# Kernel tuning notes

Hardware: AMD Instinct MI355X
Metric: run time of the kernel (lower is better)

## Reference

```python
import jax, jax.numpy as jnp
import numpy as np

EPS = 1e-5  # RMSNorm epsilon


def rmsnorm(x, w):
    return x * jax.lax.rsqrt(jnp.mean(x * x, axis=-1, keepdims=True) + EPS) * w


def mamba_forward(u, in_proj_w, conv_w, conv_b, x_proj_w, dt_proj_w, dt_proj_b,
                  A_log, D_param, mamba_out_w):
    # u: (b, L, dm) -- canonical Mamba block (expand=2, d_state=16, d_conv=4)
    b, L, dm = u.shape
    di, ds = A_log.shape
    dtr = dt_proj_w.shape[1]
    xz = jnp.einsum('bld,ed->ble', u, in_proj_w)          # (b,L,2*di)
    x_, z = jnp.split(xz, 2, axis=-1)                     # each (b,L,di)
    # causal depthwise conv over the sequence axis
    dconv = conv_w.shape[-1]
    xc = jnp.transpose(x_, (0, 2, 1))                     # (b,di,L)
    xc = jnp.pad(xc, ((0, 0), (0, 0), (dconv - 1, 0)))
    xc = jax.lax.conv_general_dilated(xc, conv_w, window_strides=(1,), padding='VALID',
                                      dimension_numbers=('NCH', 'OIH', 'NCH'),
                                      feature_group_count=di)
    xc = xc + conv_b[None, :, None]
    x_ = jax.nn.silu(jnp.transpose(xc, (0, 2, 1)))        # (b,L,di)
    # input-dependent dt, B, C
    x_dbl = jnp.einsum('bld,ed->ble', x_, x_proj_w)       # (b,L,dtr+2*ds)
    dt, B, C = jnp.split(x_dbl, [dtr, dtr + ds], axis=-1)
    delta = jax.nn.softplus(jnp.einsum('blr,dr->bld', dt, dt_proj_w) + dt_proj_b)  # (b,L,di)
    A = -jnp.exp(A_log)                                   # (di,ds)

    def step(h, inp):
        d_t, B_t, C_t, x_t = inp                          # (b,di),(b,ds),(b,ds),(b,di)
        dA = jnp.exp(d_t[:, :, None] * A)                 # (b,di,ds)
        h = dA * h + (d_t * x_t)[:, :, None] * B_t[:, None, :]
        y = jnp.einsum('bds,bs->bd', h, C_t)
        return h, y

    xs = (jnp.moveaxis(delta, 1, 0), jnp.moveaxis(B, 1, 0),
          jnp.moveaxis(C, 1, 0), jnp.moveaxis(x_, 1, 0))
    h0 = jnp.zeros((b, di, ds), dtype=u.dtype)
    _, ys = jax.lax.scan(step, h0, xs)                    # ys: (L,b,di)
    y = jnp.moveaxis(ys, 0, 1) + x_ * D_param             # (b,L,di)
    y = y * jax.nn.silu(z)
    return jnp.einsum('bld,od->blo', y, mamba_out_w)      # (b,L,dm)


def conv1x1(W, bvec, t):
    # t: (b, cin, L) -> (b, cout, L)
    return jnp.einsum('oi,bit->bot', W, t) + bvec[None, :, None]


def reference(x, w_norm1, w_norm2, W_ip, b_ip, W_fp, b_fp, W_wp, b_wp, W_op, b_op,
              in_proj_w, conv_w, conv_b, x_proj_w, dt_proj_w, dt_proj_b,
              A_log, D_param, mamba_out_w):
    # x: (b, L, D) -- module's (b, c, l) with l == input_dim = D, c == seq = L
    residual = x
    xn = rmsnorm(x, w_norm1)                 # RMSNorm over last (input_dim) axis
    xt = jnp.transpose(xn, (0, 2, 1))        # 'b c l -> b l c' : (b, D, L)
    ssm = conv1x1(W_ip, b_ip, xt)            # (b, 2D, L)
    ssm = conv1x1(W_fp, b_fp, ssm)           # (b, 2D, L)
    u = jnp.transpose(ssm, (0, 2, 1))        # (b, L, 2D): seq=L, d_model=2D
    m = mamba_forward(u, in_proj_w, conv_w, conv_b, x_proj_w, dt_proj_w, dt_proj_b,
                      A_log, D_param, mamba_out_w)
    m = rmsnorm(m, w_norm2) + u              # PostNormMamba residual
    ssm = jnp.transpose(m, (0, 2, 1))        # (b, 2D, L)
    w = conv1x1(W_wp, b_wp, xt)              # (b, 2D, L)
    w = w * jax.nn.sigmoid(w)                # swish
    out = conv1x1(W_op, b_op, w * ssm)       # (b, D, L)
    return jnp.transpose(out, (0, 2, 1)) + residual


def setup_inputs():
    key = jax.random.key(0)
    ks = jax.random.split(key, 16)
    D, L, b = 64, 4096, 4
    dm, di, ds, dconv = 2 * D, 4 * D, 16, 4
    dtr = (dm + 15) // 16  # dt_rank = ceil(d_model/16) = 8

    def n(k, shape, fan_in):
        return jax.random.normal(k, shape, jnp.float32) * (1.0 / np.sqrt(fan_in))

    return {
        'x': jax.random.normal(ks[0], (b, L, D), jnp.float32),
        'w_norm1': jnp.ones((D,), jnp.float32),
        'w_norm2': jnp.ones((dm,), jnp.float32),
        'W_ip': n(ks[1], (2 * D, D), D), 'b_ip': jnp.zeros((2 * D,), jnp.float32),
        'W_fp': n(ks[2], (2 * D, 2 * D), 2 * D), 'b_fp': jnp.zeros((2 * D,), jnp.float32),
        'W_wp': n(ks[3], (2 * D, D), D), 'b_wp': jnp.zeros((2 * D,), jnp.float32),
        'W_op': n(ks[4], (D, 2 * D), 2 * D), 'b_op': jnp.zeros((D,), jnp.float32),
        'in_proj_w': n(ks[5], (2 * di, dm), dm),
        'conv_w': n(ks[6], (di, 1, dconv), dconv),
        'conv_b': jnp.zeros((di,), jnp.float32),
        'x_proj_w': n(ks[7], (dtr + 2 * ds, di), di),
        'dt_proj_w': n(ks[8], (di, dtr), dtr),
        'dt_proj_b': jnp.full((di,), float(np.log(np.expm1(0.01))), jnp.float32),
        'A_log': jnp.log(jnp.broadcast_to(jnp.arange(1, ds + 1, dtype=jnp.float32), (di, ds))),
        'D_param': jnp.ones((di,), jnp.float32),
        'mamba_out_w': n(ks[9], (dm, di), di),
    }
```

## Files before the change

### kernel.cpp

```cpp
#include <hip/hip_runtime.h>
#include <hip/hip_bf16.h>

typedef __hip_bfloat16 bf16;
typedef __attribute__((ext_vector_type(8))) short bf16x8;
typedef __attribute__((ext_vector_type(4))) float f32x4;
#define DEV __device__ __forceinline__

constexpr int SEQ  = 4096;
constexpr int NB   = 4;
constexpr int NTOK = NB * SEQ;
constexpr float EPS = 1e-5f;
constexpr int NCH = 64;
constexpr int NCHUNK = SEQ / NCH;
constexpr float LOG2E = 1.44269504f;

constexpr int OFF_WDT  = 0;
constexpr int OFF_WB   = 2048;
constexpr int WB_IP = 0;
constexpr int WB_WP = 8192;
constexpr int WB_FP = 16384;
constexpr int WB_PR = 32768;
constexpr int WB_MO = 98304;
constexpr int WB_OP = 131072;
constexpr int WB_XP = 139264;
constexpr int WB_TOT = 151552;
constexpr int OFF_XDBL = OFF_WB + WB_TOT / 2;
constexpr int OFF_R1   = OFF_XDBL + NTOK * 40;
constexpr int OFF_WSW  = OFF_R1   + 1048576;
constexpr int OFF_U    = OFF_WSW  + 1048576;
constexpr int OFF_R2   = OFF_U    + 1048576;
constexpr int OFF_SILUZ= OFF_R2   + 2097152;
constexpr int OFF_XC   = OFF_SILUZ+ 2097152;
constexpr int OFF_G    = OFF_XC   + 2097152;
constexpr int OFF_FLAG = OFF_G    + 2097152;

DEV float b2f(bf16 x) { return __bfloat162float(x); }
DEV bf16 f2b(float x) { return __float2bfloat16(x); }
DEV short shof(bf16 h) { short s; __builtin_memcpy(&s, &h, 2); return s; }
DEV float ldin(const void* p, int i, int f) {
  return f ? ((const float*)p)[i] : b2f(((const bf16*)p)[i]);
}
DEV unsigned pack2(float a, float b) {
  bf16 ha = f2b(a), hb = f2b(b);
  unsigned short ua, ub;
  __builtin_memcpy(&ua, &ha, 2); __builtin_memcpy(&ub, &hb, 2);
  return (unsigned)ua | ((unsigned)ub << 16);
}
DEV float lo16f(unsigned u) { return __int_as_float((int)(u << 16)); }
DEV float hi16f(unsigned u) { return __int_as_float((int)(u & 0xffff0000u)); }
template<int CTRL>
DEV float dpp_add(float v) {
  int r = __builtin_amdgcn_update_dpp(0, __float_as_int(v), CTRL, 0xF, 0xF, false);
  return v + __int_as_float(r);
}
DEV float exp2f_fast(float a) { return __builtin_amdgcn_exp2f(a); }
DEV float softplus(float a) {
  return (a > 20.f) ? a : __logf(1.f + exp2f_fast(a * LOG2E));
}
DEV float silu(float a) { return a / (1.f + __expf(-a)); }

DEV void cpw(int e, int base, int count, const void* __restrict__ src,
             bf16* __restrict__ wb, int f) {
  int r = e - base;
  if (r >= 0 && r < count) wb[base + r] = f2b(ldin(src, r, f));
}
__global__ __launch_bounds__(256) void prep_k(
    const void* __restrict__ w_ip, const void* __restrict__ w_wp, const void* __restrict__ w_fp,
    const void* __restrict__ w_pr, const void* __restrict__ w_mo, const void* __restrict__ w_op,
    const void* __restrict__ w_x,  const void* __restrict__ w_dt,
    const void* __restrict__ x, float* __restrict__ wsf, int* __restrict__ flagp)
{
  __shared__ int cnt;
  if (threadIdx.x == 0) cnt = 0;
  __syncthreads();
  {
    float v = b2f(((const bf16*)x)[threadIdx.x]);
    int ok = (v == v) && fabsf(v) > 1e-4f && fabsf(v) < 100.f;
    atomicAdd(&cnt, ok);
  }
  __syncthreads();
  int f = (cnt > 204) ? 0 : 1;
  if (blockIdx.x == 0 && threadIdx.x == 0) *flagp = f;

  int e = blockIdx.x * 256 + threadIdx.x;
  bf16* wb = (bf16*)(wsf + OFF_WB);
  cpw(e, WB_IP, 8192,  w_ip, wb, f);
  cpw(e, WB_WP, 8192,  w_wp, wb, f);
  cpw(e, WB_FP, 16384, w_fp, wb, f);
  cpw(e, WB_PR, 65536, w_pr, wb, f);
  cpw(e, WB_MO, 32768, w_mo, wb, f);
  cpw(e, WB_OP, 8192,  w_op, wb, f);
  {
    int r = e - WB_XP;
    if (r >= 0 && r < 12288) wb[WB_XP + r] = (r < 10240) ? f2b(ldin(w_x, r, f)) : f2b(0.f);
  }
  if (e < 2048) {
    int r = e >> 8, d = e & 255;
    wsf[OFF_WDT + e] = ldin(w_dt, d * 8 + r, f);
  }
}

__global__ __launch_bounds__(256) void fm_k(
    const void* __restrict__ x, const void* __restrict__ w1, const float* __restrict__ wsf,
    const void* __restrict__ b_ip, const void* __restrict__ b_wp, const void* __restrict__ b_fp,
    bf16* __restrict__ wsw, bf16* __restrict__ u, bf16* __restrict__ xpre,
    bf16* __restrict__ siluz, const int* __restrict__ flagp)
{
  __shared__ short xn[32 * 72];
  __shared__ short t1[32 * 136];
  __shared__ short ul[32 * 136];
  const int f = *flagp;
  const int tid = threadIdx.x;
  const int tok0 = blockIdx.x * 32;
  {
    const int token = tid >> 3, r = tid & 7;
    float v[8]; float ss = 0.f;
    #pragma unroll
    for (int k = 0; k < 8; ++k) {
      v[k] = ldin(x, (tok0 + token) * 64 + r * 8 + k, f);
      ss += v[k] * v[k];
    }
    ss += __shfl_xor(ss, 1, 8); ss += __shfl_xor(ss, 2, 8); ss += __shfl_xor(ss, 4, 8);
    float sc = rsqrtf(ss * (1.f / 64.f) + EPS);
    unsigned* dst = (unsigned*)xn + token * 36 + r * 4;
    #pragma unroll
    for (int k = 0; k < 4; ++k) {
      int i = r * 8 + k * 2;
      dst[k] = pack2(v[k*2] * sc * ldin(w1, i, f), v[k*2+1] * sc * ldin(w1, i + 1, f));
    }
  }
  __syncthreads();
  const int lane = tid & 63, m = lane & 15, q = lane >> 4;
  const int w = tid >> 6;
  {
    const int wt = w >> 1, ng = w & 1;
    const bf16* W = (const bf16*)(wsf + OFF_WB) + (wt ? WB_WP : WB_IP);
    const void* bia = wt ? b_wp : b_ip;
    bf16x8 a[2][2];
    #pragma unroll
    for (int mt = 0; mt < 2; ++mt)
      #pragma unroll
      for (int kk = 0; kk < 2; ++kk)
        a[mt][kk] = *(const bf16x8*)&xn[(mt * 16 + m) * 72 + kk * 32 + q * 8];
    #pragma unroll
    for (int nti = 0; nti < 4; ++nti) {
      int nt = ng * 4 + nti;
      int n = nt * 16 + m;
      f32x4 acc[2] = {{0,0,0,0},{0,0,0,0}};
      #pragma unroll
      for (int kk = 0; kk < 2; ++kk) {
        bf16x8 b = *(const bf16x8*)(W + (nt * 16 + m) * 64 + kk * 32 + q * 8);
        #pragma unroll
        for (int mt = 0; mt < 2; ++mt)
          acc[mt] = __builtin_amdgcn_mfma_f32_16x16x32_bf16(a[mt][kk], b, acc[mt], 0, 0, 0);
      }
      float bv = ldin(bia, n, f);
      #pragma unroll
      for (int mt = 0; mt < 2; ++mt)
        #pragma unroll
        for (int r = 0; r < 4; ++r) {
          float v = acc[mt][r] + bv;
          if (wt) wsw[(tok0 + mt * 16 + q * 4 + r) * 128 + n] = f2b(silu(v));
          else    t1[(mt * 16 + q * 4 + r) * 136 + n] = shof(f2b(v));
        }
    }
  }
  __syncthreads();
  {
    const bf16* WF = (const bf16*)(wsf + OFF_WB) + WB_FP;
    bf16x8 a[2][4];
    #pragma unroll
    for (int mt = 0; mt < 2; ++mt)
      #pragma unroll
      for (int kk = 0; kk < 4; ++kk)
        a[mt][kk] = *(const bf16x8*)&t1[(mt * 16 + m) * 136 + kk * 32 + q * 8];
    #pragma unroll
    for (int nti = 0; nti < 2; ++nti) {
      int nt = w * 2 + nti;
      int n = nt * 16 + m;
      f32x4 acc[2] = {{0,0,0,0},{0,0,0,0}};
      #pragma unroll
      for (int kk = 0; kk < 4; ++kk) {
        bf16x8 b = *(const bf16x8*)(WF + (nt * 16 + m) * 128 + kk * 32 + q * 8);
        #pragma unroll
        for (int mt = 0; mt < 2; ++mt)
          acc[mt] = __builtin_amdgcn_mfma_f32_16x16x32_bf16(a[mt][kk], b, acc[mt], 0, 0, 0);
      }
      float bv = ldin(b_fp, n, f);
      #pragma unroll
      for (int mt = 0; mt < 2; ++mt)
        #pragma unroll
        for (int r = 0; r < 4; ++r) {
          bf16 h = f2b(acc[mt][r] + bv);
          ul[(mt * 16 + q * 4 + r) * 136 + n] = shof(h);
          u[(tok0 + mt * 16 + q * 4 + r) * 128 + n] = h;
        }
    }
  }
  __syncthreads();
  {
    const bf16* WP = (const bf16*)(wsf + OFF_WB) + WB_PR;
    bf16x8 a[2][4];
    #pragma unroll
    for (int mt = 0; mt < 2; ++mt)
      #pragma unroll
      for (int kk = 0; kk < 4; ++kk)
        a[mt][kk] = *(const bf16x8*)&ul[(mt * 16 + m) * 136 + kk * 32 + q * 8];
    #pragma unroll
    for (int nti = 0; nti < 8; ++nti) {
      int nt = w * 8 + nti;
      int n = nt * 16 + m;
      f32x4 acc[2] = {{0,0,0,0},{0,0,0,0}};
      #pragma unroll
      for (int kk = 0; kk < 4; ++kk) {
        bf16x8 b = *(const bf16x8*)(WP + (nt * 16 + m) * 128 + kk * 32 + q * 8);
        #pragma unroll
        for (int mt = 0; mt < 2; ++mt)
          acc[mt] = __builtin_amdgcn_mfma_f32_16x16x32_bf16(a[mt][kk], b, acc[mt], 0, 0, 0);
      }
      #pragma unroll
      for (int mt = 0; mt < 2; ++mt)
        #pragma unroll
        for (int r = 0; r < 4; ++r) {
          int tok = tok0 + mt * 16 + q * 4 + r;
          if (n < 256) xpre[tok * 256 + n] = f2b(acc[mt][r]);
          else         siluz[tok * 256 + (n - 256)] = f2b(silu(acc[mt][r]));
        }
    }
  }
}

__global__ __launch_bounds__(256) void conv_k(
    const bf16* __restrict__ xpre, const void* __restrict__ cw, const void* __restrict__ cb,
    const float* __restrict__ wsf, bf16* __restrict__ xc, float* __restrict__ xdbl,
    const int* __restrict__ flagp)
{
  __shared__ short xh[35 * 256];
  __shared__ short cs[32 * 264];
  const int f = *flagp;
  const int tid = threadIdx.x;
  const int tok0 = blockIdx.x * 32;
  const bool seqstart = (tok0 & (SEQ - 1)) == 0;
  for (int c = tid; c < 1120; c += 256) {
    int e0 = c * 8;
    int tt = e0 >> 8, i = e0 & 255;
    int gtok = tok0 + tt - 3;
    uint4* dst = (uint4*)(xh + e0);
    if (gtok >= 0 && !(seqstart && tt < 3)) *dst = *(const uint4*)(xpre + gtok * 256 + i);
    else                                    *dst = make_uint4(0, 0, 0, 0);
  }
  __syncthreads();
  {
    const int ch0 = (tid & 63) * 4;
    const int t0 = (tid >> 6) * 8;
    float w4[4][4], cb4[4];
    #pragma unroll
    for (int c = 0; c < 4; ++c) {
      cb4[c] = ldin(cb, ch0 + c, f);
      #pragma unroll
      for (int k = 0; k < 4; ++k) w4[c][k] = ldin(cw, (ch0 + c) * 4 + k, f);
    }
    float win[11][4];
    #pragma unroll
    for (int r = 0; r < 11; ++r) {
      uint2 v = *(const uint2*)&xh[(t0 + r) * 256 + ch0];
      win[r][0] = lo16f(v.x); win[r][1] = hi16f(v.x);
      win[r][2] = lo16f(v.y); win[r][3] = hi16f(v.y);
    }
    #pragma unroll
    for (int t = 0; t < 8; ++t) {
      unsigned pk[2];
      #pragma unroll
      for (int cp = 0; cp < 2; ++cp) {
        float o[2];
        #pragma unroll
        for (int ci = 0; ci < 2; ++ci) {
          int c = cp * 2 + ci;
          float acc = cb4[c];
          #pragma unroll
          for (int k = 0; k < 4; ++k) acc = fmaf(win[t + k][c], w4[c][k], acc);
          o[ci] = silu(acc);
        }
        pk[cp] = pack2(o[0], o[1]);
      }
      uint2 pv = make_uint2(pk[0], pk[1]);
      *(uint2*)&cs[(t0 + t) * 264 + ch0] = pv;
      *(uint2*)(xc + (tok0 + t0 + t) * 256 + ch0) = pv;
    }
  }
  __syncthreads();
  const int w = tid >> 6;
  if (w < 2) {
    const bf16* Wx = (const bf16*)(wsf + OFF_WB) + WB_XP;
    const int lane = tid & 63, m = lane & 15, quad = lane >> 4;
    f32x4 acc[3] = {{0,0,0,0},{0,0,0,0},{0,0,0,0}};
    #pragma unroll
    for (int k0 = 0; k0 < 256; k0 += 32) {
      bf16x8 af = *(const bf16x8*)&cs[(w * 16 + m) * 264 + k0 + quad * 8];
      #pragma unroll
      for (int nt = 0; nt < 3; ++nt) {
        bf16x8 bfr = *(const bf16x8*)(Wx + (nt * 16 + m) * 256 + k0 + quad * 8);
        acc[nt] = __builtin_amdgcn_mfma_f32_16x16x32_bf16(af, bfr, acc[nt], 0, 0, 0);
      }
    }
    #pragma unroll
    for (int nt = 0; nt < 3; ++nt) {
      int n = nt * 16 + m;
      if (n < 40) {
        #pragma unroll
        for (int r = 0; r < 4; ++r)
          xdbl[(tok0 + w * 16 + quad * 4 + r) * 40 + n] = acc[nt][r];
      }
    }
  }
}

template<bool IS_C>
__global__ __launch_bounds__(256) void scan_k(
    const float* __restrict__ xdbl, const bf16* __restrict__ xc, const bf16* __restrict__ siluz,
    const void* __restrict__ A_log, const void* __restrict__ D_par, const void* __restrict__ dt_b,
    const float* __restrict__ WDT, float* __restrict__ summ, const float* __restrict__ hinit,
    bf16* __restrict__ g, const int* __restrict__ flagp)
{
  const int f = *flagp;
  const int tid = threadIdx.x;
  const int bb = blockIdx.x >> 4, dg = blockIdx.x & 15, c = blockIdx.y;
  const int dl = tid >> 4, s = tid & 15;
  const int j = s;
  const int d_loop = dg * 16 + dl;
  const int d_stg  = dg * 16 + j;
  const int tok_base = bb * SEQ + c * NCH;

  __shared__ float dt_l[NCH * 8];
  __shared__ float dx_l[NCH * 16 * 2];
  __shared__ float bc_l[IS_C ? NCH * 16 * 2 : NCH * 16];
  __shared__ float g_l[IS_C ? NCH * 16 : 1];

  const float Aval2 = -__expf(ldin(A_log, d_loop * 16 + s, f)) * LOG2E;
  const float Dp_stg = ldin(D_par, d_stg, f);
  const float dtb_j = ldin(dt_b, d_stg, f);
  float wdt[8];
  #pragma unroll
  for (int r = 0; r < 8; ++r) wdt[r] = WDT[r * 256 + d_stg];

  const int sidx = (blockIdx.x * NCHUNK + c) * 256 + tid;
  float h = IS_C ? hinit[sidx] : 0.f;
  float sdlt = 0.f;

  for (int e2 = tid * 4; e2 < NCH * 8; e2 += 1024)
    *(float4*)(dt_l + e2) = *(const float4*)(xdbl + (tok_base + (e2 >> 3)) * 40 + (e2 & 7));
  #pragma unroll
  for (int k = 0; k < 4; ++k) {
    int e = tid + k * 256;
    int t = e >> 4;
    int tok = tok_base + t;
    float B = xdbl[tok * 40 + 8 + j];
    if (IS_C) {
      bc_l[e * 2 + 0] = B;
      bc_l[e * 2 + 1] = xdbl[tok * 40 + 24 + j];
    } else bc_l[e] = B;
  }
  __syncthreads();
  #pragma unroll
  for (int k = 0; k < 4; ++k) {
    int e = tid + k * 256;
    int t = e >> 4;
    float a = dtb_j;
    #pragma unroll
    for (int r = 0; r < 8; ++r) a = fmaf(dt_l[t * 8 + r], wdt[r], a);
    float dlt = softplus(a);
    float xcv = b2f(xc[(tok_base + t) * 256 + d_stg]);
    *(float2*)(dx_l + e * 2) = make_float2(dlt, dlt * xcv);
  }
  __syncthreads();

  #pragma unroll 8
  for (int t = 0; t < NCH; ++t) {
    float2 dx = *(const float2*)(dx_l + (t * 16 + dl) * 2);
    float dA = exp2f_fast(dx.x * Aval2);
    if (!IS_C) sdlt += dx.x;
    if (IS_C) {
      float2 bc = *(const float2*)(bc_l + (t * 16 + s) * 2);
      h = fmaf(dA, h, dx.y * bc.x);
      float p = h * bc.y;
      p = dpp_add<0x121>(p);
      p = dpp_add<0x122>(p);
      p = dpp_add<0x124>(p);
      p = dpp_add<0x128>(p);
      if (s == 0) g_l[t * 16 + dl] = p;
    } else {
      h = fmaf(dA, h, dx.y * bc_l[t * 16 + s]);
    }
  }
  if (IS_C) {
    __syncthreads();
    #pragma unroll
    for (int k = 0; k < 4; ++k) {
      int e = tid + k * 256;
      int t = e >> 4;
      int tok = tok_base + t;
      float xcv = b2f(xc[tok * 256 + d_stg]);
      g[tok * 256 + d_stg] = f2b((g_l[e] + xcv * Dp_stg) * b2f(siluz[tok * 256 + d_stg]));
    }
  } else {
    *(float2*)(summ + sidx * 2) = make_float2(exp2f_fast(Aval2 * sdlt), h);
  }
}

__global__ __launch_bounds__(256) void scanB_k(const float* __restrict__ summ, float* __restrict__ hinit) {
  int bx = blockIdx.x, qq = threadIdx.x;
  float h = 0.f;
  for (int c0 = 0; c0 < NCHUNK; c0 += 16) {
    float2 sv[16];
    #pragma unroll
    for (int k = 0; k < 16; ++k)
      sv[k] = *(const float2*)(summ + ((bx * NCHUNK + c0 + k) * 256 + qq) * 2);
    #pragma unroll
    for (int k = 0; k < 16; ++k) {
      hinit[(bx * NCHUNK + c0 + k) * 256 + qq] = h;
      h = fmaf(sv[k].x, h, sv[k].y);
    }
  }
}

__global__ __launch_bounds__(256) void back_k(
    const bf16* __restrict__ g, const float* __restrict__ wsf, const void* __restrict__ w2,
    const bf16* __restrict__ u, const bf16* __restrict__ wsw, const void* __restrict__ b_op,
    const void* __restrict__ x, void* __restrict__ out, const int* __restrict__ flagp)
{
  __shared__ short ms[32 * 136];
  const int f = *flagp;
  const int tid = threadIdx.x;
  const int tok0 = blockIdx.x * 32;
  const int lane = tid & 63, m = lane & 15, q = lane >> 4;
  const int w = tid >> 6;
  const bf16* WM = (const bf16*)(wsf + OFF_WB) + WB_MO;
  const bf16* WO = (const bf16*)(wsf + OFF_WB) + WB_OP;
  {
    f32x4 acc[2][2] = {{{0,0,0,0},{0,0,0,0}},{{0,0,0,0},{0,0,0,0}}};
    #pragma unroll
    for (int kk = 0; kk < 8; ++kk) {
      bf16x8 a0 = *(const bf16x8*)(g + (tok0 + m) * 256 + kk * 32 + q * 8);
      bf16x8 a1 = *(const bf16x8*)(g + (tok0 + 16 + m) * 256 + kk * 32 + q * 8);
      #pragma unroll
      for (int nti = 0; nti < 2; ++nti) {
        int nt = w * 2 + nti;
        bf16x8 b = *(const bf16x8*)(WM + (nt * 16 + m) * 256 + kk * 32 + q * 8);
        acc[nti][0] = __builtin_amdgcn_mfma_f32_16x16x32_bf16(a0, b, acc[nti][0], 0, 0, 0);
        acc[nti][1] = __builtin_amdgcn_mfma_f32_16x16x32_bf16(a1, b, acc[nti][1], 0, 0, 0);
      }
    }
    #pragma unroll
    for (int nti = 0; nti < 2; ++nti) {
      int n = (w * 2 + nti) * 16 + m;
      #pragma unroll
      for (int mt = 0; mt < 2; ++mt)
        #pragma unroll
        for (int r = 0; r < 4; ++r)
          ms[(mt * 16 + q * 4 + r) * 136 + n] = shof(f2b(acc[nti][mt][r]));
    }
  }
  __syncthreads();
  {
    const int token = tid >> 3, r = tid & 7;
    float mv[16]; float ss = 0.f;
    #pragma unroll
    for (int k = 0; k < 16; ++k) {
      mv[k] = b2f(((const bf16*)ms)[token * 136 + r * 16 + k]);
      ss += mv[k] * mv[k];
    }
    ss += __shfl_xor(ss, 1, 8); ss += __shfl_xor(ss, 2, 8); ss += __shfl_xor(ss, 4, 8);
    float sc = rsqrtf(ss * (1.f / 128.f) + EPS);
    #pragma unroll
    for (int k = 0; k < 16; ++k) {
      int i = r * 16 + k;
      int ga = (tok0 + token) * 128 + i;
      float v = mv[k] * sc * ldin(w2, i, f) + b2f(u[ga]);
      ms[token * 136 + i] = shof(f2b(v * b2f(wsw[ga])));
    }
  }
  __syncthreads();
  {
    bf16x8 a[2][4];
    #pragma unroll
    for (int mt = 0; mt < 2; ++mt)
      #pragma unroll
      for (int kk = 0; kk < 4; ++kk)
        a[mt][kk] = *(const bf16x8*)&ms[(mt * 16 + m) * 136 + kk * 32 + q * 8];
    int nt = w;
    f32x4 acc[2] = {{0,0,0,0},{0,0,0,0}};
    #pragma unroll
    for (int kk = 0; kk < 4; ++kk) {
      bf16x8 b = *(const bf16x8*)(WO + (nt * 16 + m) * 128 + kk * 32 + q * 8);
      #pragma unroll
      for (int mt = 0; mt < 2; ++mt)
        acc[mt] = __builtin_amdgcn_mfma_f32_16x16x32_bf16(a[mt][kk], b, acc[mt], 0, 0, 0);
    }
    int n = nt * 16 + m;
    float bv = ldin(b_op, n, f);
    #pragma unroll
    for (int mt = 0; mt < 2; ++mt)
      #pragma unroll
      for (int r = 0; r < 4; ++r) {
        int token = tok0 + mt * 16 + q * 4 + r;
        float v = acc[mt][r] + bv + ldin(x, token * 64 + n, f);
        if (f) ((float*)out)[token * 64 + n] = v;
        else   ((bf16*)out)[token * 64 + n] = f2b(v);
      }
  }
}

extern "C" void kernel_launch(void* const* d_in, const int* in_sizes, int n_in,
                              void* d_out, int out_size, void* d_ws, size_t ws_size,
                              hipStream_t stream) {
  (void)in_sizes; (void)n_in; (void)out_size; (void)ws_size;
  const void* x        = d_in[0];
  const void* w_norm1  = d_in[1];
  const void* w_norm2  = d_in[2];
  const void* W_ip     = d_in[3];
  const void* b_ip     = d_in[4];
  const void* W_fp     = d_in[5];
  const void* b_fp     = d_in[6];
  const void* W_wp     = d_in[7];
  const void* b_wp     = d_in[8];
  const void* W_op     = d_in[9];
  const void* b_op     = d_in[10];
  const void* in_proj  = d_in[11];
  const void* conv_w   = d_in[12];
  const void* conv_b   = d_in[13];
  const void* x_proj   = d_in[14];
  const void* dt_projw = d_in[15];
  const void* dt_projb = d_in[16];
  const void* A_log    = d_in[17];
  const void* D_par    = d_in[18];
  const void* mo_w     = d_in[19];

  float* wsf    = (float*)d_ws;
  float* xdbl   = wsf + OFF_XDBL;
  float* hin    = wsf + OFF_R1;
  bf16*  wsw_b  = (bf16*)(wsf + OFF_WSW);
  bf16*  u_b    = (bf16*)(wsf + OFF_U);
  bf16*  xpre_b = (bf16*)(wsf + OFF_R2);
  float* summ   = wsf + OFF_R2;
  bf16*  siluz_b= (bf16*)(wsf + OFF_SILUZ);
  bf16*  xc_b   = (bf16*)(wsf + OFF_XC);
  bf16*  g_b    = (bf16*)(wsf + OFF_G);
  int*   flagp  = (int*)(wsf + OFF_FLAG);

  prep_k<<<dim3(592), dim3(256), 0, stream>>>(W_ip, W_wp, W_fp, in_proj, mo_w, W_op,
                                              x_proj, dt_projw, x, wsf, flagp);
  fm_k<<<dim3(NTOK / 32), dim3(256), 0, stream>>>(x, w_norm1, wsf, b_ip, b_wp, b_fp,
                                                  wsw_b, u_b, xpre_b, siluz_b, flagp);
  conv_k<<<dim3(NTOK / 32), dim3(256), 0, stream>>>(xpre_b, conv_w, conv_b, wsf, xc_b, xdbl, flagp);
  scan_k<false><<<dim3(64, NCHUNK), dim3(256), 0, stream>>>(xdbl, xc_b, siluz_b, A_log, D_par,
                                                            dt_projb, wsf + OFF_WDT, summ, hin, g_b, flagp);
  scanB_k<<<dim3(64), dim3(256), 0, stream>>>(summ, hin);
  scan_k<true><<<dim3(64, NCHUNK), dim3(256), 0, stream>>>(xdbl, xc_b, siluz_b, A_log, D_par,
                                                           dt_projb, wsf + OFF_WDT, summ, hin, g_b, flagp);
  back_k<<<dim3(NTOK / 32), dim3(256), 0, stream>>>(g_b, wsf, w_norm2, u_b, wsw_b, b_op, x, d_out, flagp);
}
```

Measured before the change: 210.7 us.

## Fuse chunk-state combine into scan pass via last-block atomic counter

Removes the separate scanB_k launch that combines per-chunk scan summaries. Each first-pass scan block now increments a per-(batch, d-group) atomic counter after a threadfence, and the last block to arrive serially combines all chunk summaries into hinit. prep_k zeros the 64 counters each run. This saves one kernel launch and its gap, but the final serial combine now runs inside the tail of a single block, and correctness depends on the memory fences and on the counters being reset.

```diff
diff --git a/kernel.cpp b/kernel.cpp
--- a/kernel.cpp
+++ b/kernel.cpp
@@ -81,6 +81,7 @@
   __syncthreads();
   int f = (cnt > 204) ? 0 : 1;
   if (blockIdx.x == 0 && threadIdx.x == 0) *flagp = f;
+  if (blockIdx.x == 0 && threadIdx.x < 64) flagp[1 + threadIdx.x] = 0;
 
   int e = blockIdx.x * 256 + threadIdx.x;
   bf16* wb = (bf16*)(wsf + OFF_WB);
@@ -319,8 +320,8 @@
 __global__ __launch_bounds__(256) void scan_k(
     const float* __restrict__ xdbl, const bf16* __restrict__ xc, const bf16* __restrict__ siluz,
     const void* __restrict__ A_log, const void* __restrict__ D_par, const void* __restrict__ dt_b,
-    const float* __restrict__ WDT, float* __restrict__ summ, const float* __restrict__ hinit,
-    bf16* __restrict__ g, const int* __restrict__ flagp)
+    const float* __restrict__ WDT, float* __restrict__ summ, float* __restrict__ hinit,
+    bf16* __restrict__ g, const int* __restrict__ flagp, int* __restrict__ cnt)
 {
   const int f = *flagp;
   const int tid = threadIdx.x;
@@ -335,6 +336,7 @@
   __shared__ float dx_l[NCH * 16 * 2];
   __shared__ float bc_l[IS_C ? NCH * 16 * 2 : NCH * 16];
   __shared__ float g_l[IS_C ? NCH * 16 : 1];
+  __shared__ int lastflag;
 
   const float Aval2 = -__expf(ldin(A_log, d_loop * 16 + s, f)) * LOG2E;
   const float Dp_stg = ldin(D_par, d_stg, f);
@@ -404,21 +406,28 @@
     }
   } else {
     *(float2*)(summ + sidx * 2) = make_float2(exp2f_fast(Aval2 * sdlt), h);
-  }
-}
-
-__global__ __launch_bounds__(256) void scanB_k(const float* __restrict__ summ, float* __restrict__ hinit) {
-  int bx = blockIdx.x, qq = threadIdx.x;
-  float h = 0.f;
-  for (int c0 = 0; c0 < NCHUNK; c0 += 16) {
-    float2 sv[16];
-    #pragma unroll
-    for (int k = 0; k < 16; ++k)
-      sv[k] = *(const float2*)(summ + ((bx * NCHUNK + c0 + k) * 256 + qq) * 2);
-    #pragma unroll
-    for (int k = 0; k < 16; ++k) {
-      hinit[(bx * NCHUNK + c0 + k) * 256 + qq] = h;
-      h = fmaf(sv[k].x, h, sv[k].y);
+    __threadfence();
+    __syncthreads();
+    if (tid == 0) {
+      int old = atomicAdd(&cnt[blockIdx.x], 1);
+      lastflag = (old == NCHUNK - 1);
+    }
+    __syncthreads();
+    if (lastflag) {
+      __threadfence();
+      const int bx = blockIdx.x, qq = tid;
+      float hh = 0.f;
+      for (int c0 = 0; c0 < NCHUNK; c0 += 16) {
+        float2 sv[16];
+        #pragma unroll
+        for (int k = 0; k < 16; ++k)
+          sv[k] = *(const float2*)(summ + ((bx * NCHUNK + c0 + k) * 256 + qq) * 2);
+        #pragma unroll
+        for (int k = 0; k < 16; ++k) {
+          hinit[(bx * NCHUNK + c0 + k) * 256 + qq] = hh;
+          hh = fmaf(sv[k].x, hh, sv[k].y);
+        }
+      }
     }
   }
 }
@@ -546,6 +555,7 @@
   bf16*  xc_b   = (bf16*)(wsf + OFF_XC);
   bf16*  g_b    = (bf16*)(wsf + OFF_G);
   int*   flagp  = (int*)(wsf + OFF_FLAG);
+  int*   cntp   = flagp + 1;
 
   prep_k<<<dim3(592), dim3(256), 0, stream>>>(W_ip, W_wp, W_fp, in_proj, mo_w, W_op,
                                               x_proj, dt_projw, x, wsf, flagp);
@@ -553,9 +563,8 @@
                                                   wsw_b, u_b, xpre_b, siluz_b, flagp);
   conv_k<<<dim3(NTOK / 32), dim3(256), 0, stream>>>(xpre_b, conv_w, conv_b, wsf, xc_b, xdbl, flagp);
   scan_k<false><<<dim3(64, NCHUNK), dim3(256), 0, stream>>>(xdbl, xc_b, siluz_b, A_log, D_par,
-                                                            dt_projb, wsf + OFF_WDT, summ, hin, g_b, flagp);
-  scanB_k<<<dim3(64), dim3(256), 0, stream>>>(summ, hin);
+                                                            dt_projb, wsf + OFF_WDT, summ, hin, g_b, flagp, cntp);
   scan_k<true><<<dim3(64, NCHUNK), dim3(256), 0, stream>>>(xdbl, xc_b, siluz_b, A_log, D_par,
-                                                           dt_projb, wsf + OFF_WDT, summ, hin, g_b, flagp);
+                                                           dt_projb, wsf + OFF_WDT, summ, hin, g_b, flagp, cntp);
   back_k<<<dim3(NTOK / 32), dim3(256), 0, stream>>>(g_b, wsf, w_norm2, u_b, wsw_b, b_op, x, d_out, flagp);
 }
```

Measured after the change: 538.0 us. 155% more time.
